# Kernel optimization log

Measured on AMD Instinct MI355X. Metric: run time of the kernel, lower is better.

Reference implementation:

```python
import jax, jax.numpy as jnp
from jax import lax
import numpy as np

# dims
VOCAB = 64
B, L = 64, 2048
EMB = 128
D_MODEL = 128
N_LAYERS = 4
D_INNER = 256      # expand=2
D_STATE = 16
D_CONV = 4
DT_RANK = 8        # ceil(d_model/16)
NCLS = 3
BN_EPS = 1e-5
RMS_EPS = 1e-5


def setup_inputs():
    key = jax.random.key(0)
    ks = iter(jax.random.split(key, 48))
    def rn(shape, s=0.02):
        return jax.random.normal(next(ks), shape, jnp.float32) * s
    tokens = jax.random.randint(next(ks), (B, L), 0, VOCAB)
    mask = jnp.ones((B, L), jnp.float32)
    emb = rn((VOCAB, EMB)).at[0].set(0.0)  # padding_idx=0
    bn_w = jnp.ones((EMB,), jnp.float32)
    bn_b = jnp.zeros((EMB,), jnp.float32)
    conv_w = rn((D_MODEL, EMB, 3))
    conv_b = jnp.zeros((D_MODEL,), jnp.float32)
    in_proj_w = rn((N_LAYERS, 2 * D_INNER, D_MODEL))
    conv1d_w = rn((N_LAYERS, D_INNER, D_CONV), 0.1)
    conv1d_b = jnp.zeros((N_LAYERS, D_INNER), jnp.float32)
    x_proj_w = rn((N_LAYERS, DT_RANK + 2 * D_STATE, D_INNER))
    dt_proj_w = rn((N_LAYERS, D_INNER, DT_RANK), 0.1)
    dt_proj_b = rn((N_LAYERS, D_INNER), 0.1)
    A_log = jnp.tile(jnp.log(jnp.arange(1, D_STATE + 1, dtype=jnp.float32))[None, None, :],
                     (N_LAYERS, D_INNER, 1))
    D_param = jnp.ones((N_LAYERS, D_INNER), jnp.float32)
    out_proj_w = rn((N_LAYERS, D_MODEL, D_INNER))
    norm_w = jnp.ones((N_LAYERS, D_MODEL), jnp.float32)
    lin1_w = rn((512, D_MODEL)); lin1_b = jnp.zeros((512,), jnp.float32)
    lin2_w = rn((512, 512));     lin2_b = jnp.zeros((512,), jnp.float32)
    lin3_w = rn((NCLS, 512));    lin3_b = jnp.zeros((NCLS,), jnp.float32)
    return dict(tokens=tokens, mask=mask, emb=emb, bn_w=bn_w, bn_b=bn_b,
                conv_w=conv_w, conv_b=conv_b, in_proj_w=in_proj_w,
                conv1d_w=conv1d_w, conv1d_b=conv1d_b, x_proj_w=x_proj_w,
                dt_proj_w=dt_proj_w, dt_proj_b=dt_proj_b, A_log=A_log,
                D_param=D_param, out_proj_w=out_proj_w, norm_w=norm_w,
                lin1_w=lin1_w, lin1_b=lin1_b, lin2_w=lin2_w, lin2_b=lin2_b,
                lin3_w=lin3_w, lin3_b=lin3_b)


def _rmsnorm(x, w):
    return x * lax.rsqrt(jnp.mean(x * x, axis=-1, keepdims=True) + RMS_EPS) * w


def _selective_scan(u, dt, A, Bm, Cm, Dv):
    # u, dt: (B,L,di); A: (di,ds); Bm, Cm: (B,L,ds); Dv: (di,)
    def step(h, inp):
        dt_t, B_t, C_t, u_t = inp           # (B,di),(B,ds),(B,ds),(B,di)
        dA = jnp.exp(dt_t[:, :, None] * A)  # (B,di,ds)
        h = dA * h + (dt_t * u_t)[:, :, None] * B_t[:, None, :]
        y = jnp.einsum('bds,bs->bd', h, C_t)
        return h, y
    h0 = jnp.zeros((u.shape[0], A.shape[0], A.shape[1]), u.dtype)
    xs = (jnp.swapaxes(dt, 0, 1), jnp.swapaxes(Bm, 0, 1),
          jnp.swapaxes(Cm, 0, 1), jnp.swapaxes(u, 0, 1))
    _, ys = lax.scan(step, h0, xs)          # ys: (L,B,di)
    return jnp.swapaxes(ys, 0, 1) + u * Dv


def _mamba(x, in_w, cw, cb, xp_w, dtp_w, dtp_b, A_log, Dv, out_w):
    # x: (B,L,d_model)
    xz = jnp.einsum('bld,ed->ble', x, in_w)            # (B,L,2*di)
    xi, z = jnp.split(xz, 2, axis=-1)
    # causal depthwise conv over time
    xc = jnp.swapaxes(xi, 1, 2)                        # (B,di,L)
    xc = lax.conv_general_dilated(xc, cw[:, None, :], (1,), [(D_CONV - 1, 0)],
                                  dimension_numbers=('NCH', 'OIH', 'NCH'),
                                  feature_group_count=D_INNER)
    xc = jax.nn.silu(xc + cb[None, :, None])
    xc = jnp.swapaxes(xc, 1, 2)                        # (B,L,di)
    x_dbl = jnp.einsum('bld,ed->ble', xc, xp_w)        # (B,L,dtr+2*ds)
    dt = jax.nn.softplus(jnp.einsum('blr,dr->bld', x_dbl[..., :DT_RANK], dtp_w) + dtp_b)
    Bm = x_dbl[..., DT_RANK:DT_RANK + D_STATE]
    Cm = x_dbl[..., DT_RANK + D_STATE:]
    A = -jnp.exp(A_log)                                # (di,ds)
    y = _selective_scan(xc, dt, A, Bm, Cm, Dv)
    y = y * jax.nn.silu(z)
    return jnp.einsum('ble,de->bld', y, out_w)         # (B,L,d_model)


def _forward(tokens, mask, emb, bn_w, bn_b, conv_w, conv_b, in_proj_w,
             conv1d_w, conv1d_b, x_proj_w, dt_proj_w, dt_proj_b, A_log,
             D_param, out_proj_w, norm_w, lin1_w, lin1_b, lin2_w, lin2_b,
             lin3_w, lin3_b):
    x = emb[tokens]                                    # (B,L,E)
    xc = jnp.swapaxes(x, 1, 2)                         # (B,E,L)
    # BatchNorm1d in eval mode: running_mean=0, running_var=1
    xc = xc * (bn_w * lax.rsqrt(jnp.array(1.0 + BN_EPS)))[None, :, None] + bn_b[None, :, None]
    xc = lax.conv_general_dilated(xc, conv_w, (1,), [(1, 1)],
                                  dimension_numbers=('NCH', 'OIH', 'NCH'))
    xc = jax.nn.relu(xc + conv_b[None, :, None])
    x = jnp.swapaxes(xc, 1, 2)                         # (B,L,D_MODEL)
    for i in range(N_LAYERS):
        x = _mamba(_rmsnorm(x, norm_w[i]), in_proj_w[i], conv1d_w[i],
                   conv1d_b[i], x_proj_w[i], dt_proj_w[i], dt_proj_b[i],
                   A_log[i], D_param[i], out_proj_w[i]) + x
    # masked average pooling
    m = mask[:, :, None]
    denom = jnp.clip(jnp.sum(m, axis=1), 1e-9, None)   # (B,1)->(B,D) broadcast
    pooled = jnp.sum(x * m, axis=1) / denom
    h = jax.nn.relu(pooled @ lin1_w.T + lin1_b)
    h = jax.nn.relu(h @ lin2_w.T + lin2_b)
    return h @ lin3_w.T + lin3_b                       # (B,NCLS)


def reference(tokens, mask, emb, bn_w, bn_b, conv_w, conv_b, in_proj_w,
              conv1d_w, conv1d_b, x_proj_w, dt_proj_w, dt_proj_b, A_log,
              D_param, out_proj_w, norm_w, lin1_w, lin1_b, lin2_w, lin2_b,
              lin3_w, lin3_b):
    return _forward(tokens, mask, emb, bn_w, bn_b, conv_w, conv_b, in_proj_w,
                    conv1d_w, conv1d_b, x_proj_w, dt_proj_w, dt_proj_b, A_log,
                    D_param, out_proj_w, norm_w, lin1_w, lin1_b, lin2_w,
                    lin2_b, lin3_w, lin3_b)
```

## Files before the change

### kernel.cpp

```cpp
#include <hip/hip_runtime.h>
#include <math.h>

#define NB     64
#define SL     2048
#define NTOK   (NB*SL)
#define EMB_D  128
#define DMODEL 128
#define DIN    256
#define DST    16
#define NLAYER 4
#define SEG    64
#define NSEG   (SL/SEG)
#define L2E    1.4426950408889634f
#define LN2    0.6931471805599453f

typedef __bf16 bf16x8 __attribute__((ext_vector_type(8)));
typedef __bf16 bf16x4 __attribute__((ext_vector_type(4)));
typedef float  f32x4  __attribute__((ext_vector_type(4)));

#define FIX_PL   ((size_t)0)
#define FIX_PM   (FIX_PL + 131072)
#define FIX_PD   (FIX_PM + 1024)
#define FIX_H1   (FIX_PD + 8192)
#define FIX_H2   (FIX_H1 + 32768)
#define FIX_WP   (FIX_H2 + 32768)
#define FIX_W2B  (FIX_WP + 65536)
#define FIX_WINB (FIX_W2B + 24576)
#define FIX_WOUTB (FIX_WINB + 131072)
#define FIX_END  (FIX_WOUTB + 65536)

__device__ __forceinline__ float fexp2(float x){ return __builtin_amdgcn_exp2f(x); }
__device__ __forceinline__ float flog2(float x){ return __builtin_amdgcn_logf(x); }
__device__ __forceinline__ float frcp (float x){ return __builtin_amdgcn_rcpf(x); }
__device__ __forceinline__ float fast_exp(float x){ return fexp2(x*L2E); }
__device__ __forceinline__ float siluf(float v){ return v * frcp(1.f + fast_exp(-v)); }
__device__ __forceinline__ float softplusf(float a){
  return fmaxf(a,0.f) + flog2(1.f + fexp2(-fabsf(a)*L2E)) * LN2;
}
__device__ __forceinline__ unsigned short bfbits(float x){
  __bf16 b = (__bf16)x; return __builtin_bit_cast(unsigned short, b);
}
__device__ __forceinline__ unsigned int packdu(float dt, float u){
  return ((unsigned int)bfbits(u) << 16) | (unsigned int)bfbits(dt);
}

#define SPSA(hA,hB,q,s0,s1) { float eA=fexp2(dt*(-fast_exp(alog[d*DST+s0])*L2E)); \
                              hA=fmaf(eA,hA,du*q.x); \
                              float eB=fexp2(dt*(-fast_exp(alog[d*DST+s1])*L2E)); \
                              hB=fmaf(eB,hB,du*q.z); }
#define SPSY(hA,hB,q,s0,s1) { float eA=fexp2(dt*(-fast_exp(alog[d*DST+s0])*L2E)); \
                              hA=fmaf(eA,hA,du*q.x); y=fmaf(hA,q.y,y); \
                              float eB=fexp2(dt*(-fast_exp(alog[d*DST+s1])*L2E)); \
                              hB=fmaf(eB,hB,du*q.z); y=fmaf(hB,q.w,y); }

#define POWTREE(r) \
  float r2=(r)*(r), r4=r2*r2, r8=r4*r4; \
  float r3=r2*(r), r5=r4*(r), r6=r4*r2, r7=r4*r3; \
  float r9=r8*(r), r10=r8*r2, r11=r8*r3, r12=r8*r4; \
  float r13=r8*r5, r14=r8*r6, r15=r8*r7, r16=r8*r8;

__global__ void k_w2b(const float* __restrict__ cw, __bf16* __restrict__ w2){
  int g = blockIdx.x*256 + threadIdx.x;
  if (g >= 128*384) return;
  int d = g / 384, j = g % 384;
  int k = j >> 7, e = j & 127;
  w2[d*384 + k*128 + e] = (__bf16)cw[d*384 + e*3 + k];
}

__global__ void k_cvt(const float* __restrict__ src, __bf16* __restrict__ dst, int n){
  int i = blockIdx.x*256 + threadIdx.x;
  if (i < n) dst[i] = (__bf16)src[i];
}

__global__ void k_wprep(const float* __restrict__ xpw, __bf16* __restrict__ wp){
  int g = blockIdx.x*256 + threadIdx.x;
  int l = g >> 14, rem = g & 16383;
  int n = rem >> 8, k = rem & 255;
  float v = 0.f;
  if (n < 8){
    v = xpw[(size_t)l*40*256 + n*256 + k];
  } else if (n < 40){
    int i = n - 8;
    int row = 8 + ((i&1)<<4) + (i>>1);
    v = xpw[(size_t)l*40*256 + row*256 + k];
  }
  wp[g] = (__bf16)v;
}

__global__ void k_embed(const int* __restrict__ tok, const float* __restrict__ emb,
                        const float* __restrict__ bnw, const float* __restrict__ bnb,
                        float* __restrict__ xp){
  int r = blockIdx.x;
  int e = threadIdx.x;
  int b = r / 2050, tp = r % 2050;
  float v = 0.f;
  if (tp != 0 && tp != 2049){
    int t = tp - 1;
    int id = tok[(size_t)b*SL + t];
    float s = bnw[e] * rsqrtf(1.0f + 1e-5f);
    v = emb[(size_t)id*EMB_D + e] * s + bnb[e];
  }
  xp[(size_t)r*EMB_D + e] = v;
}

__global__ __launch_bounds__(256) void k_rmsscale(const float* __restrict__ x,
                                                  float* __restrict__ rs){
  int wv = threadIdx.x>>6, lane = threadIdx.x&63;
  size_t tok = (size_t)blockIdx.x*4 + wv;
  float2 v = *(const float2*)(x + tok*128 + lane*2);
  float ss = v.x*v.x + v.y*v.y;
  #pragma unroll
  for (int m=1;m<64;m<<=1) ss += __shfl_xor(ss, m);
  float r = rsqrtf(ss*(1.f/128.f) + 1e-5f);
  if (lane == 0) rs[tok] = r;
}

template<int MODE, int K, int N>
__global__ __launch_bounds__(256) void k_mgemm(
    const void* __restrict__ Av, const __bf16* __restrict__ Wb,
    const float* __restrict__ bias, const float* __restrict__ rsp,
    const float* __restrict__ nwp,
    float* __restrict__ out, __bf16* __restrict__ outb, __bf16* __restrict__ outz){
  __shared__ __bf16 As[128][40];
  __shared__ __bf16 Bs[128][40];
  const int tid  = threadIdx.x;
  const int wave = tid >> 6;
  const int lane = tid & 63;
  const int col  = lane & 15;
  const int quad = lane >> 4;
  const int wm = (wave & 1) * 64;
  const int wn = (wave >> 1) * 64;
  const int m0 = blockIdx.y * 128;
  const int n0 = blockIdx.x * 128;

  f32x4 acc[4][4];
  #pragma unroll
  for (int i=0;i<4;i++)
    #pragma unroll
    for (int j=0;j<4;j++) acc[i][j] = (f32x4){0.f,0.f,0.f,0.f};

  size_t abase;
  if constexpr(MODE==0){
    int bb = m0 >> 11, tloc = m0 & 2047;
    abase = ((size_t)bb*2050 + tloc) * 128;
  } else {
    abase = (size_t)m0 * K;
  }

  const int sm = tid >> 3;
  const int sk4 = (tid & 7) * 4;
  const int bn = tid >> 2;
  const int bk8 = (tid & 3) * 8;

  for (int k0 = 0; k0 < K; k0 += 32){
    #pragma unroll
    for (int p=0;p<4;p++){
      int m = p*32 + sm;
      const float* A = (const float*)Av;
      float4 v;
      if constexpr(MODE==0){
        v = *(const float4*)(A + abase + (size_t)m*128 + k0 + sk4);
      } else {
        float4 x4 = *(const float4*)(A + abase + (size_t)m*K + k0 + sk4);
        float4 w4 = *(const float4*)(nwp + k0 + sk4);
        float s = rsp[m0 + m];
        v.x = x4.x*s*w4.x; v.y = x4.y*s*w4.y; v.z = x4.z*s*w4.z; v.w = x4.w*s*w4.w;
      }
      bf16x4 o;
      o[0] = (__bf16)v.x; o[1] = (__bf16)v.y; o[2] = (__bf16)v.z; o[3] = (__bf16)v.w;
      *(bf16x4*)&As[m][sk4] = o;
    }
    #pragma unroll
    for (int p=0;p<2;p++){
      int n = p*64 + bn;
      bf16x8 w = *(const bf16x8*)(Wb + (size_t)(n0+n)*K + k0 + bk8);
      *(bf16x8*)&Bs[n][bk8] = w;
    }
    __syncthreads();
    bf16x8 af[4], bfr[4];
    const int fq = quad*8;
    #pragma unroll
    for (int i=0;i<4;i++) af[i]  = *(const bf16x8*)&As[wm + i*16 + col][fq];
    #pragma unroll
    for (int j=0;j<4;j++) bfr[j] = *(const bf16x8*)&Bs[wn + j*16 + col][fq];
    #pragma unroll
    for (int i=0;i<4;i++)
      #pragma unroll
      for (int j=0;j<4;j++)
        acc[i][j] = __builtin_amdgcn_mfma_f32_16x16x32_bf16(af[i], bfr[j], acc[i][j], 0, 0, 0);
    __syncthreads();
  }

  #pragma unroll
  for (int i=0;i<4;i++){
    #pragma unroll
    for (int j=0;j<4;j++){
      int n_l = wn + j*16 + col;
      #pragma unroll
      for (int r=0;r<4;r++){
        int m = m0 + wm + i*16 + quad*4 + r;
        float c = acc[i][j][r];
        if constexpr(MODE==0){
          int n = n0 + n_l;
          out[(size_t)m*DMODEL + n] = fmaxf(c + bias[n], 0.f);
        } else {
          int n = n0 + n_l;
          if (n < DIN) outb[(size_t)m*DIN + n]        = (__bf16)c;
          else         outz[(size_t)m*DIN + n - DIN]  = (__bf16)siluf(c);
        }
      }
    }
  }
}

__global__ __launch_bounds__(256) void k_seg(const __bf16* __restrict__ xi,
    const __bf16* __restrict__ wpb,
    const float* __restrict__ cw, const float* __restrict__ cb,
    const float* __restrict__ dtw, const float* __restrict__ dtb,
    const float* __restrict__ alog,
    float* __restrict__ vbc, unsigned int* __restrict__ dub,
    float* __restrict__ cseg, float* __restrict__ sdtb){
  __shared__ __bf16 sxc[64][264];
  __shared__ float vls[64][68];
  const int tid = threadIdx.x;
  const size_t m0 = (size_t)blockIdx.x * 64;
  const int b = (int)(m0 >> 11);
  const int g = (int)((m0 >> 6) & (NSEG-1));
  const int seq0 = (int)(m0 & 2047);

  {
    const int c4 = (tid & 63) * 4;
    const int tw = tid >> 6;
    float wc[4][4];
    #pragma unroll
    for (int j=0;j<4;j++)
      #pragma unroll
      for (int k=0;k<4;k++) wc[j][k] = cw[(c4+j)*4 + k];
    float4 cb4 = *(const float4*)(cb + c4);
    #pragma unroll
    for (int it=0; it<16; it++){
      int t = it*4 + tw;
      float4 acc = cb4;
      #pragma unroll
      for (int k=0;k<4;k++){
        if (seq0 + t - 3 + k >= 0){
          bf16x4 xv = *(const bf16x4*)(xi + (m0 + t - 3 + k)*DIN + c4);
          acc.x = fmaf(wc[0][k], (float)xv[0], acc.x);
          acc.y = fmaf(wc[1][k], (float)xv[1], acc.y);
          acc.z = fmaf(wc[2][k], (float)xv[2], acc.z);
          acc.w = fmaf(wc[3][k], (float)xv[3], acc.w);
        }
      }
      bf16x4 o;
      o[0]=(__bf16)siluf(acc.x); o[1]=(__bf16)siluf(acc.y);
      o[2]=(__bf16)siluf(acc.z); o[3]=(__bf16)siluf(acc.w);
      *(bf16x4*)&sxc[t][c4] = o;
    }
  }
  __syncthreads();

  {
    const int wave = tid >> 6, lane = tid & 63;
    const int col = lane & 15, quad = lane >> 4;
    const int wn = wave * 16;
    f32x4 acc[4];
    #pragma unroll
    for (int i=0;i<4;i++) acc[i] = (f32x4){0.f,0.f,0.f,0.f};
    #pragma unroll
    for (int kc=0;kc<8;kc++){
      bf16x8 bfr = *(const bf16x8*)(wpb + (size_t)(wn+col)*256 + kc*32 + quad*8);
      #pragma unroll
      for (int mi=0;mi<4;mi++){
        bf16x8 af = *(const bf16x8*)&sxc[mi*16 + col][kc*32 + quad*8];
        acc[mi] = __builtin_amdgcn_mfma_f32_16x16x32_bf16(af, bfr, acc[mi], 0, 0, 0);
      }
    }
    #pragma unroll
    for (int mi=0;mi<4;mi++)
      #pragma unroll
      for (int r=0;r<4;r++)
        vls[mi*16 + quad*4 + r][wn + col] = acc[mi][r];
  }
  __syncthreads();

  #pragma unroll
  for (int p=0;p<8;p++){
    int j = p*256 + tid;
    int t = j >> 5, i = j & 31;
    vbc[(m0+t)*32 + i] = vls[t][8+i];
  }

  {
    const int d = tid;
    const float a0 = -fast_exp(alog[d*DST]) * L2E;
    bool fast = true;
    for (int s=1;s<16;s++){
      float as = -fast_exp(alog[d*DST + s]) * L2E;
      fast = fast && (fabsf(as - (float)(s+1)*a0) <= 1e-3f*fabsf(as));
    }
    float4 w8a = *(const float4*)(dtw + d*8);
    float4 w8b = *(const float4*)(dtw + d*8 + 4);
    const float bd = dtb[d];
    float h0=0.f,h1=0.f,h2=0.f,h3=0.f,h4=0.f,h5=0.f,h6=0.f,h7=0.f;
    float h8=0.f,h9=0.f,h10=0.f,h11=0.f,h12=0.f,h13=0.f,h14=0.f,h15=0.f;
    float ssum = 0.f;
    if (fast){
      for (int t=0;t<SEG;t++){
        float4 v0 = *(const float4*)&vls[t][0];
        float4 v1 = *(const float4*)&vls[t][4];
        float lin = bd;
        lin = fmaf(v0.x,w8a.x, fmaf(v0.y,w8a.y, fmaf(v0.z,w8a.z, fmaf(v0.w,w8a.w, lin))));
        lin = fmaf(v1.x,w8b.x, fmaf(v1.y,w8b.y, fmaf(v1.z,w8b.z, fmaf(v1.w,w8b.w, lin))));
        float dt = softplusf(lin);
        ssum += dt;
        float u = (float)sxc[t][d];
        dub[(m0+t)*DIN + d] = packdu(dt, u);
        float du = dt*u;
        float r1 = fexp2(dt*a0);
        POWTREE(r1)
        float4 q0 = *(const float4*)&vls[t][8];
        float4 q1 = *(const float4*)&vls[t][12];
        float4 q2 = *(const float4*)&vls[t][16];
        float4 q3 = *(const float4*)&vls[t][20];
        float4 q4 = *(const float4*)&vls[t][24];
        float4 q5 = *(const float4*)&vls[t][28];
        float4 q6 = *(const float4*)&vls[t][32];
        float4 q7 = *(const float4*)&vls[t][36];
        h0 =fmaf(r1 ,h0 ,du*q0.x); h1 =fmaf(r2 ,h1 ,du*q0.z);
        h2 =fmaf(r3 ,h2 ,du*q1.x); h3 =fmaf(r4 ,h3 ,du*q1.z);
        h4 =fmaf(r5 ,h4 ,du*q2.x); h5 =fmaf(r6 ,h5 ,du*q2.z);
        h6 =fmaf(r7 ,h6 ,du*q3.x); h7 =fmaf(r8 ,h7 ,du*q3.z);
        h8 =fmaf(r9 ,h8 ,du*q4.x); h9 =fmaf(r10,h9 ,du*q4.z);
        h10=fmaf(r11,h10,du*q5.x); h11=fmaf(r12,h11,du*q5.z);
        h12=fmaf(r13,h12,du*q6.x); h13=fmaf(r14,h13,du*q6.z);
        h14=fmaf(r15,h14,du*q7.x); h15=fmaf(r16,h15,du*q7.z);
      }
    } else {
      for (int t=0;t<SEG;t++){
        float4 v0 = *(const float4*)&vls[t][0];
        float4 v1 = *(const float4*)&vls[t][4];
        float lin = bd;
        lin = fmaf(v0.x,w8a.x, fmaf(v0.y,w8a.y, fmaf(v0.z,w8a.z, fmaf(v0.w,w8a.w, lin))));
        lin = fmaf(v1.x,w8b.x, fmaf(v1.y,w8b.y, fmaf(v1.z,w8b.z, fmaf(v1.w,w8b.w, lin))));
        float dt = softplusf(lin);
        ssum += dt;
        float u = (float)sxc[t][d];
        dub[(m0+t)*DIN + d] = packdu(dt, u);
        float du = dt*u;
        float4 q0 = *(const float4*)&vls[t][8];
        float4 q1 = *(const float4*)&vls[t][12];
        float4 q2 = *(const float4*)&vls[t][16];
        float4 q3 = *(const float4*)&vls[t][20];
        float4 q4 = *(const float4*)&vls[t][24];
        float4 q5 = *(const float4*)&vls[t][28];
        float4 q6 = *(const float4*)&vls[t][32];
        float4 q7 = *(const float4*)&vls[t][36];
        SPSA(h0,h1,q0,0,1)   SPSA(h2,h3,q1,2,3)   SPSA(h4,h5,q2,4,5)   SPSA(h6,h7,q3,6,7)
        SPSA(h8,h9,q4,8,9)   SPSA(h10,h11,q5,10,11) SPSA(h12,h13,q6,12,13) SPSA(h14,h15,q7,14,15)
      }
    }
    size_t base = (((size_t)b*NSEG + g)*DIN + d)*DST;
    float4 o;
    o.x=h0; o.y=h1; o.z=h2; o.w=h3;     *(float4*)(cseg + base     ) = o;
    o.x=h4; o.y=h5; o.z=h6; o.w=h7;     *(float4*)(cseg + base +  4) = o;
    o.x=h8; o.y=h9; o.z=h10; o.w=h11;   *(float4*)(cseg + base +  8) = o;
    o.x=h12; o.y=h13; o.z=h14; o.w=h15; *(float4*)(cseg + base + 12) = o;
    sdtb[((size_t)b*NSEG + g)*DIN + d] = ssum;
  }
}

__global__ __launch_bounds__(256) void k_scanB(float* __restrict__ cseg,
    const float* __restrict__ sdtb, const float* __restrict__ alog){
  int gl = blockIdx.x*256 + threadIdx.x;
  int b   = gl >> 12;
  int rem = gl & 4095;
  int d = rem >> 4, s = rem & 15;
  const float a = -fast_exp(alog[d*DST + s]) * L2E;
  float h = 0.f;
  for (int g=0; g<NSEG; g++){
    size_t base = ((size_t)b*NSEG + g)*DIN;
    float sd = sdtb[base + d];
    size_t ci = (base + d)*DST + s;
    float c = cseg[ci];
    cseg[ci] = h;
    h = fmaf(fexp2(a*sd), h, c);
  }
}

__global__ __launch_bounds__(256) void k_scanC3(float* __restrict__ xres,
    const unsigned int* __restrict__ dub, const float* __restrict__ vbc,
    const __bf16* __restrict__ gzb,
    const float* __restrict__ alog, const float* __restrict__ Dpar,
    const float* __restrict__ cseg, const __bf16* __restrict__ wout,
    float* __restrict__ rs){
  __shared__ __bf16 sy[64][264];
  __shared__ float svbc[64][32];
  float* sx = (float*)sy;
  const int tid = threadIdx.x;
  const size_t m0 = (size_t)blockIdx.x * 64;
  const int b = (int)(m0 >> 11);
  const int g = (int)((m0 >> 6) & (NSEG-1));

  #pragma unroll
  for (int p=0;p<8;p++){
    int j = p*256 + tid;
    int t = j >> 5, i = j & 31;
    svbc[t][i] = vbc[(m0+t)*32 + i];
  }

  {
    const int d = tid;
    const float a0 = -fast_exp(alog[d*DST]) * L2E;
    bool fast = true;
    for (int s=1;s<16;s++){
      float as = -fast_exp(alog[d*DST + s]) * L2E;
      fast = fast && (fabsf(as - (float)(s+1)*a0) <= 1e-3f*fabsf(as));
    }
    const float Dv = Dpar[d];
    size_t base = (((size_t)b*NSEG + g)*DIN + d)*DST;
    float4 hv0 = *(const float4*)(cseg + base);
    float4 hv1 = *(const float4*)(cseg + base + 4);
    float4 hv2 = *(const float4*)(cseg + base + 8);
    float4 hv3 = *(const float4*)(cseg + base + 12);
    float h0=hv0.x,h1=hv0.y,h2=hv0.z,h3=hv0.w;
    float h4=hv1.x,h5=hv1.y,h6=hv1.z,h7=hv1.w;
    float h8=hv2.x,h9=hv2.y,h10=hv2.z,h11=hv2.w;
    float h12=hv3.x,h13=hv3.y,h14=hv3.z,h15=hv3.w;
    __syncthreads();

    if (fast){
      unsigned int w = dub[m0*DIN + d];
      float gz = (float)gzb[m0*DIN + d];
      for (int t=0;t<SEG;t++){
        int tn = (t < SEG-1) ? t+1 : t;
        unsigned int wn_ = dub[(m0+tn)*DIN + d];
        float gzn = (float)gzb[(m0+tn)*DIN + d];
        float u  = __builtin_bit_cast(float, w & 0xffff0000u);
        float dt = __builtin_bit_cast(float, w << 16);
        float du = dt*u;
        float r1 = fexp2(dt*a0);
        POWTREE(r1)
        float4 q0 = *(const float4*)&svbc[t][0];
        float4 q1 = *(const float4*)&svbc[t][4];
        float4 q2 = *(const float4*)&svbc[t][8];
        float4 q3 = *(const float4*)&svbc[t][12];
        float4 q4 = *(const float4*)&svbc[t][16];
        float4 q5 = *(const float4*)&svbc[t][20];
        float4 q6 = *(const float4*)&svbc[t][24];
        float4 q7 = *(const float4*)&svbc[t][28];
        h0 =fmaf(r1 ,h0 ,du*q0.x); h1 =fmaf(r2 ,h1 ,du*q0.z);
        h2 =fmaf(r3 ,h2 ,du*q1.x); h3 =fmaf(r4 ,h3 ,du*q1.z);
        h4 =fmaf(r5 ,h4 ,du*q2.x); h5 =fmaf(r6 ,h5 ,du*q2.z);
        h6 =fmaf(r7 ,h6 ,du*q3.x); h7 =fmaf(r8 ,h7 ,du*q3.z);
        h8 =fmaf(r9 ,h8 ,du*q4.x); h9 =fmaf(r10,h9 ,du*q4.z);
        h10=fmaf(r11,h10,du*q5.x); h11=fmaf(r12,h11,du*q5.z);
        h12=fmaf(r13,h12,du*q6.x); h13=fmaf(r14,h13,du*q6.z);
        h14=fmaf(r15,h14,du*q7.x); h15=fmaf(r16,h15,du*q7.z);
        float ya = fmaf(h0,q0.y, fmaf(h1,q0.w, fmaf(h2,q1.y, h3*q1.w)));
        float yb = fmaf(h4,q2.y, fmaf(h5,q2.w, fmaf(h6,q3.y, h7*q3.w)));
        float yc = fmaf(h8,q4.y, fmaf(h9,q4.w, fmaf(h10,q5.y, h11*q5.w)));
        float yd = fmaf(h12,q6.y, fmaf(h13,q6.w, fmaf(h14,q7.y, h15*q7.w)));
        float y = (ya+yb)+(yc+yd);
        sy[t][d] = (__bf16)((y + u*Dv) * gz);
        w = wn_; gz = gzn;
      }
    } else {
      for (int t=0;t<SEG;t++){
        unsigned int w = dub[(m0+t)*DIN + d];
        float u  = __builtin_bit_cast(float, w & 0xffff0000u);
        float dt = __builtin_bit_cast(float, w << 16);
        float du = dt*u;
        float y = 0.f;
        float4 q0 = *(const float4*)&svbc[t][0];
        float4 q1 = *(const float4*)&svbc[t][4];
        float4 q2 = *(const float4*)&svbc[t][8];
        float4 q3 = *(const float4*)&svbc[t][12];
        float4 q4 = *(const float4*)&svbc[t][16];
        float4 q5 = *(const float4*)&svbc[t][20];
        float4 q6 = *(const float4*)&svbc[t][24];
        float4 q7 = *(const float4*)&svbc[t][28];
        SPSY(h0,h1,q0,0,1)   SPSY(h2,h3,q1,2,3)   SPSY(h4,h5,q2,4,5)   SPSY(h6,h7,q3,6,7)
        SPSY(h8,h9,q4,8,9)   SPSY(h10,h11,q5,10,11) SPSY(h12,h13,q6,12,13) SPSY(h14,h15,q7,14,15)
        float gz = (float)gzb[(m0+t)*DIN + d];
        sy[t][d] = (__bf16)((y + u*Dv) * gz);
      }
    }
  }
  __syncthreads();

  const int wave = tid >> 6, lane = tid & 63;
  const int col = lane & 15, quad = lane >> 4;
  const int wn = wave * 32;
  f32x4 acc[4][2];
  #pragma unroll
  for (int i=0;i<4;i++)
    #pragma unroll
    for (int j=0;j<2;j++) acc[i][j] = (f32x4){0.f,0.f,0.f,0.f};
  #pragma unroll
  for (int kc=0;kc<8;kc++){
    bf16x8 bfr0 = *(const bf16x8*)(wout + (size_t)(wn +      col)*256 + kc*32 + quad*8);
    bf16x8 bfr1 = *(const bf16x8*)(wout + (size_t)(wn + 16 + col)*256 + kc*32 + quad*8);
    #pragma unroll
    for (int mi=0;mi<4;mi++){
      bf16x8 af = *(const bf16x8*)&sy[mi*16 + col][kc*32 + quad*8];
      acc[mi][0] = __builtin_amdgcn_mfma_f32_16x16x32_bf16(af, bfr0, acc[mi][0], 0, 0, 0);
      acc[mi][1] = __builtin_amdgcn_mfma_f32_16x16x32_bf16(af, bfr1, acc[mi][1], 0, 0, 0);
    }
  }
  __syncthreads();

  #pragma unroll
  for (int mi=0;mi<4;mi++){
    #pragma unroll
    for (int j=0;j<2;j++){
      int n = wn + j*16 + col;
      #pragma unroll
      for (int r=0;r<4;r++){
        int ml = mi*16 + quad*4 + r;
        size_t go = (m0 + ml)*DMODEL + n;
        float nx = xres[go] + acc[mi][j][r];
        xres[go] = nx;
        sx[ml*132 + n] = nx;
      }
    }
  }
  __syncthreads();
  {
    int row = tid >> 2, q = tid & 3;
    const float* pr = sx + row*132 + q*32;
    float ss = 0.f;
    #pragma unroll
    for (int i=0;i<32;i+=4){
      float4 v = *(const float4*)(pr + i);
      ss += v.x*v.x + v.y*v.y + v.z*v.z + v.w*v.w;
    }
    ss += __shfl_xor(ss, 1);
    ss += __shfl_xor(ss, 2);
    if (q == 0) rs[m0 + row] = rsqrtf(ss*(1.f/128.f) + 1e-5f);
  }
}

__global__ __launch_bounds__(256) void k_pool1(const float* __restrict__ x,
    const float* __restrict__ mask, float* __restrict__ part, float* __restrict__ pmask){
  int b = blockIdx.y, seg = blockIdx.x;
  int d = threadIdx.x & 127, half = threadIdx.x >> 7;
  int t0 = seg*128 + half*64;
  float acc = 0.f, macc = 0.f;
  for (int i=0;i<64;i++){
    int t = t0 + i;
    float mv = mask[(size_t)b*SL + t];
    acc = fmaf(x[((size_t)b*SL + t)*DMODEL + d], mv, acc);
    macc += mv;
  }
  __shared__ float sm[256];
  __shared__ float smm[2];
  sm[threadIdx.x] = acc;
  if (d == 0) smm[half] = macc;
  __syncthreads();
  if (half == 0){
    part[((size_t)b*16 + seg)*128 + d] = sm[d] + sm[128+d];
    if (d == 0) pmask[b*16 + seg] = smm[0] + smm[1];
  }
}

__global__ void k_pool2(const float* __restrict__ part, const float* __restrict__ pmask,
                        float* __restrict__ pooled){
  int b = blockIdx.x, d = threadIdx.x;
  float acc = 0.f, ms = 0.f;
  for (int s=0;s<16;s++){ acc += part[((size_t)b*16+s)*128 + d]; ms += pmask[b*16+s]; }
  pooled[(size_t)b*128 + d] = acc / fmaxf(ms, 1e-9f);
}

__global__ void k_mlp_a(const float* __restrict__ in, const float* __restrict__ w,
                        const float* __restrict__ bias, float* __restrict__ out, int K){
  int b = blockIdx.y;
  int n = blockIdx.x*128 + threadIdx.x;
  const float4* pw = (const float4*)(w + (size_t)n*K);
  const float4* pi = (const float4*)(in + (size_t)b*K);
  float acc = 0.f;
  for (int k=0;k<K/4;k++){
    float4 a = pi[k], ww = pw[k];
    acc = fmaf(a.x,ww.x, fmaf(a.y,ww.y, fmaf(a.z,ww.z, fmaf(a.w,ww.w, acc))));
  }
  out[(size_t)b*512 + n] = fmaxf(acc + bias[n], 0.f);
}

__global__ void k_mlp3(const float* __restrict__ h, const float* __restrict__ w,
                       const float* __restrict__ bias, float* __restrict__ out){
  int b = blockIdx.x;
  int n = threadIdx.x >> 6, lane = threadIdx.x & 63;
  if (n >= 3) return;
  float acc = 0.f;
  for (int k=lane; k<512; k+=64) acc = fmaf(h[(size_t)b*512+k], w[(size_t)n*512+k], acc);
  #pragma unroll
  for (int m=1;m<64;m<<=1) acc += __shfl_xor(acc, m);
  if (lane == 0) out[(size_t)b*3 + n] = acc + bias[n];
}

extern "C" void kernel_launch(void* const* d_in, const int* in_sizes, int n_in,
                              void* d_out, int out_size, void* d_ws, size_t ws_size,
                              hipStream_t stream){
  const int*   tokens = (const int*)  d_in[0];
  const float* mask   = (const float*)d_in[1];
  const float* emb    = (const float*)d_in[2];
  const float* bn_w   = (const float*)d_in[3];
  const float* bn_b   = (const float*)d_in[4];
  const float* conv_w = (const float*)d_in[5];
  const float* conv_b = (const float*)d_in[6];
  const float* in_w   = (const float*)d_in[7];
  const float* c1_w   = (const float*)d_in[8];
  const float* c1_b   = (const float*)d_in[9];
  const float* xp_w   = (const float*)d_in[10];
  const float* dtp_w  = (const float*)d_in[11];
  const float* dtp_b  = (const float*)d_in[12];
  const float* A_log  = (const float*)d_in[13];
  const float* D_par  = (const float*)d_in[14];
  const float* out_w  = (const float*)d_in[15];
  const float* nrm_w  = (const float*)d_in[16];
  const float* l1w = (const float*)d_in[17]; const float* l1b = (const float*)d_in[18];
  const float* l2w = (const float*)d_in[19]; const float* l2b = (const float*)d_in[20];
  const float* l3w = (const float*)d_in[21]; const float* l3b = (const float*)d_in[22];
  float* dout = (float*)d_out;

  int CB = 64;
  while (CB > 1 && ((size_t)CB*SL*741 + FIX_END)*4 > ws_size) CB >>= 1;
  if (((size_t)CB*SL*741 + FIX_END)*4 > ws_size) return;
  const size_t CTOK = (size_t)CB*SL;

  float* ws  = (float*)d_ws;
  float* pl  = ws + FIX_PL;
  float* pm  = ws + FIX_PM;
  float* pd  = ws + FIX_PD;
  float* h1  = ws + FIX_H1;
  float* h2  = ws + FIX_H2;
  __bf16* wpb   = (__bf16*)(ws + FIX_WP);
  __bf16* w2b   = (__bf16*)(ws + FIX_W2B);
  __bf16* winb  = (__bf16*)(ws + FIX_WINB);
  __bf16* woutb = (__bf16*)(ws + FIX_WOUTB);
  float* xcb = ws + FIX_END;
  float* rs  = xcb + CTOK*128;
  __bf16* xib = (__bf16*)(rs + CTOK);
  unsigned int* dub = (unsigned int*)(xib + CTOK*256);
  float* pad = (float*)xib;
  float* vbc = (float*)(dub + CTOK*256);
  float* csg = vbc + CTOK*32;
  float* sdt = csg + CTOK*64;
  __bf16* zb  = (__bf16*)(sdt + CTOK*4);

  k_w2b<<<192, 256, 0, stream>>>(conv_w, w2b);
  k_cvt<<<1024, 256, 0, stream>>>(in_w,  winb,  4*512*128);
  k_cvt<<<512,  256, 0, stream>>>(out_w, woutb, 4*128*256);
  k_wprep<<<256, 256, 0, stream>>>(xp_w, wpb);

  const int nchunks = NB / CB;
  for (int c = 0; c < nchunks; c++){
    const int* tok_c = tokens + (size_t)c*CTOK;

    k_embed<<<CB*2050, 128, 0, stream>>>(tok_c, emb, bn_w, bn_b, pad);
    k_mgemm<0,384,128><<<dim3(1, CTOK/128), 256, 0, stream>>>(
        pad, w2b, conv_b, nullptr, nullptr, xcb, nullptr, nullptr);
    k_rmsscale<<<CTOK/4, 256, 0, stream>>>(xcb, rs);

    for (int layer = 0; layer < NLAYER; layer++){
      const __bf16* lin = winb  + (size_t)layer*512*128;
      const float* lcw  = c1_w  + (size_t)layer*DIN*4;
      const float* lcb  = c1_b  + (size_t)layer*DIN;
      const float* ldw  = dtp_w + (size_t)layer*DIN*8;
      const float* ldb  = dtp_b + (size_t)layer*DIN;
      const float* lal  = A_log + (size_t)layer*DIN*DST;
      const float* lD   = D_par + (size_t)layer*DIN;
      const __bf16* low = woutb + (size_t)layer*128*256;
      const float* lnw  = nrm_w + (size_t)layer*128;

      k_mgemm<1,128,512><<<dim3(4, CTOK/128), 256, 0, stream>>>(
          xcb, lin, nullptr, rs, lnw, nullptr, xib, zb);
      k_seg<<<(int)(CTOK/64), 256, 0, stream>>>(
          xib, wpb + (size_t)layer*64*256, lcw, lcb, ldw, ldb, lal, vbc, dub, csg, sdt);
      k_scanB<<<CB*16, 256, 0, stream>>>(csg, sdt, lal);
      k_scanC3<<<(int)(CTOK/64), 256, 0, stream>>>(
          xcb, dub, vbc, zb, lal, lD, csg, low, rs);
    }

    k_pool1<<<dim3(16, CB), 256, 0, stream>>>(
        xcb, mask + (size_t)c*CTOK, pl + (size_t)c*CB*16*128, pm + (size_t)c*CB*16);
  }

  k_pool2<<<NB, 128, 0, stream>>>(pl, pm, pd);
  k_mlp_a<<<dim3(4, NB), 128, 0, stream>>>(pd, l1w, l1b, h1, 128);
  k_mlp_a<<<dim3(4, NB), 128, 0, stream>>>(h1, l2w, l2b, h2, 512);
  k_mlp3<<<NB, 256, 0, stream>>>(h2, l3w, l3b, dout);
}
```

Measured before the change: 1.520 ms.

## Split SSM state across two threads per channel in seg and scan kernels

Doubles the block size of k_seg and k_scanC3 to 512 threads and assigns each d_inner channel to two threads, each holding 8 of the 16 state elements. The y reduction is combined with a lane shuffle, and the MFMA and reduction work is redistributed across 8 waves. This aims to cut per-thread serial recurrence work and register pressure so more waves are resident to hide latency. In exchange it adds redundant dt/softplus computation in both halves, shuffle overhead, and half-idle lanes on the stores.

```diff
diff --git a/kernel.cpp b/kernel.cpp
--- a/kernel.cpp
+++ b/kernel.cpp
@@ -43,21 +43,6 @@
 __device__ __forceinline__ unsigned int packdu(float dt, float u){
   return ((unsigned int)bfbits(u) << 16) | (unsigned int)bfbits(dt);
 }
-
-#define SPSA(hA,hB,q,s0,s1) { float eA=fexp2(dt*(-fast_exp(alog[d*DST+s0])*L2E)); \
-                              hA=fmaf(eA,hA,du*q.x); \
-                              float eB=fexp2(dt*(-fast_exp(alog[d*DST+s1])*L2E)); \
-                              hB=fmaf(eB,hB,du*q.z); }
-#define SPSY(hA,hB,q,s0,s1) { float eA=fexp2(dt*(-fast_exp(alog[d*DST+s0])*L2E)); \
-                              hA=fmaf(eA,hA,du*q.x); y=fmaf(hA,q.y,y); \
-                              float eB=fexp2(dt*(-fast_exp(alog[d*DST+s1])*L2E)); \
-                              hB=fmaf(eB,hB,du*q.z); y=fmaf(hB,q.w,y); }
-
-#define POWTREE(r) \
-  float r2=(r)*(r), r4=r2*r2, r8=r4*r4; \
-  float r3=r2*(r), r5=r4*(r), r6=r4*r2, r7=r4*r3; \
-  float r9=r8*(r), r10=r8*r2, r11=r8*r3, r12=r8*r4; \
-  float r13=r8*r5, r14=r8*r6, r15=r8*r7, r16=r8*r8;
 
 __global__ void k_w2b(const float* __restrict__ cw, __bf16* __restrict__ w2){
   int g = blockIdx.x*256 + threadIdx.x;
@@ -213,7 +198,7 @@
   }
 }
 
-__global__ __launch_bounds__(256) void k_seg(const __bf16* __restrict__ xi,
+__global__ __launch_bounds__(512,6) void k_seg(const __bf16* __restrict__ xi,
     const __bf16* __restrict__ wpb,
     const float* __restrict__ cw, const float* __restrict__ cb,
     const float* __restrict__ dtw, const float* __restrict__ dtb,
@@ -238,8 +223,8 @@
       for (int k=0;k<4;k++) wc[j][k] = cw[(c4+j)*4 + k];
     float4 cb4 = *(const float4*)(cb + c4);
     #pragma unroll
-    for (int it=0; it<16; it++){
-      int t = it*4 + tw;
+    for (int it=0; it<8; it++){
+      int t = it*8 + tw;
       float4 acc = cb4;
       #pragma unroll
       for (int k=0;k<4;k++){
@@ -262,36 +247,38 @@
   {
     const int wave = tid >> 6, lane = tid & 63;
     const int col = lane & 15, quad = lane >> 4;
-    const int wn = wave * 16;
-    f32x4 acc[4];
-    #pragma unroll
-    for (int i=0;i<4;i++) acc[i] = (f32x4){0.f,0.f,0.f,0.f};
+    const int wr  = (wave >> 2) * 32;
+    const int wc2 = (wave & 3) * 16;
+    f32x4 acc[2];
+    acc[0] = (f32x4){0.f,0.f,0.f,0.f};
+    acc[1] = (f32x4){0.f,0.f,0.f,0.f};
     #pragma unroll
     for (int kc=0;kc<8;kc++){
-      bf16x8 bfr = *(const bf16x8*)(wpb + (size_t)(wn+col)*256 + kc*32 + quad*8);
-      #pragma unroll
-      for (int mi=0;mi<4;mi++){
-        bf16x8 af = *(const bf16x8*)&sxc[mi*16 + col][kc*32 + quad*8];
+      bf16x8 bfr = *(const bf16x8*)(wpb + (size_t)(wc2+col)*256 + kc*32 + quad*8);
+      #pragma unroll
+      for (int mi=0;mi<2;mi++){
+        bf16x8 af = *(const bf16x8*)&sxc[wr + mi*16 + col][kc*32 + quad*8];
         acc[mi] = __builtin_amdgcn_mfma_f32_16x16x32_bf16(af, bfr, acc[mi], 0, 0, 0);
       }
     }
     #pragma unroll
-    for (int mi=0;mi<4;mi++)
+    for (int mi=0;mi<2;mi++)
       #pragma unroll
       for (int r=0;r<4;r++)
-        vls[mi*16 + quad*4 + r][wn + col] = acc[mi][r];
+        vls[wr + mi*16 + quad*4 + r][wc2 + col] = acc[mi][r];
   }
   __syncthreads();
 
   #pragma unroll
-  for (int p=0;p<8;p++){
-    int j = p*256 + tid;
+  for (int p=0;p<4;p++){
+    int j = p*512 + tid;
     int t = j >> 5, i = j & 31;
     vbc[(m0+t)*32 + i] = vls[t][8+i];
   }
 
   {
-    const int d = tid;
+    const int d = tid >> 1;
+    const int half = tid & 1;
     const float a0 = -fast_exp(alog[d*DST]) * L2E;
     bool fast = true;
     for (int s=1;s<16;s++){
@@ -301,8 +288,10 @@
     float4 w8a = *(const float4*)(dtw + d*8);
     float4 w8b = *(const float4*)(dtw + d*8 + 4);
     const float bd = dtb[d];
-    float h0=0.f,h1=0.f,h2=0.f,h3=0.f,h4=0.f,h5=0.f,h6=0.f,h7=0.f;
-    float h8=0.f,h9=0.f,h10=0.f,h11=0.f,h12=0.f,h13=0.f,h14=0.f,h15=0.f;
+    const int qb = half*16;
+    float h[8];
+    #pragma unroll
+    for (int k=0;k<8;k++) h[k] = 0.f;
     float ssum = 0.f;
     if (fast){
       for (int t=0;t<SEG;t++){
@@ -314,28 +303,25 @@
         float dt = softplusf(lin);
         ssum += dt;
         float u = (float)sxc[t][d];
-        dub[(m0+t)*DIN + d] = packdu(dt, u);
+        if (!half) dub[(m0+t)*DIN + d] = packdu(dt, u);
         float du = dt*u;
         float r1 = fexp2(dt*a0);
-        POWTREE(r1)
-        float4 q0 = *(const float4*)&vls[t][8];
-        float4 q1 = *(const float4*)&vls[t][12];
-        float4 q2 = *(const float4*)&vls[t][16];
-        float4 q3 = *(const float4*)&vls[t][20];
-        float4 q4 = *(const float4*)&vls[t][24];
-        float4 q5 = *(const float4*)&vls[t][28];
-        float4 q6 = *(const float4*)&vls[t][32];
-        float4 q7 = *(const float4*)&vls[t][36];
-        h0 =fmaf(r1 ,h0 ,du*q0.x); h1 =fmaf(r2 ,h1 ,du*q0.z);
-        h2 =fmaf(r3 ,h2 ,du*q1.x); h3 =fmaf(r4 ,h3 ,du*q1.z);
-        h4 =fmaf(r5 ,h4 ,du*q2.x); h5 =fmaf(r6 ,h5 ,du*q2.z);
-        h6 =fmaf(r7 ,h6 ,du*q3.x); h7 =fmaf(r8 ,h7 ,du*q3.z);
-        h8 =fmaf(r9 ,h8 ,du*q4.x); h9 =fmaf(r10,h9 ,du*q4.z);
-        h10=fmaf(r11,h10,du*q5.x); h11=fmaf(r12,h11,du*q5.z);
-        h12=fmaf(r13,h12,du*q6.x); h13=fmaf(r14,h13,du*q6.z);
-        h14=fmaf(r15,h14,du*q7.x); h15=fmaf(r16,h15,du*q7.z);
+        float r2=r1*r1, r3=r2*r1, r4=r2*r2, r5=r4*r1, r6=r4*r2, r7=r4*r3, r8=r4*r4;
+        float bs = half ? r8 : 1.0f;
+        float4 q0 = *(const float4*)&vls[t][8+qb];
+        float4 q1 = *(const float4*)&vls[t][12+qb];
+        float4 q2 = *(const float4*)&vls[t][16+qb];
+        float4 q3 = *(const float4*)&vls[t][20+qb];
+        float pw[8] = {r1,r2,r3,r4,r5,r6,r7,r8};
+        float B_[8] = {q0.x,q0.z,q1.x,q1.z,q2.x,q2.z,q3.x,q3.z};
+        #pragma unroll
+        for (int k=0;k<8;k++)
+          h[k] = fmaf(bs*pw[k], h[k], du*B_[k]);
       }
     } else {
+      float aA[8];
+      #pragma unroll
+      for (int k=0;k<8;k++) aA[k] = -fast_exp(alog[d*DST + half*8 + k]) * L2E;
       for (int t=0;t<SEG;t++){
         float4 v0 = *(const float4*)&vls[t][0];
         float4 v1 = *(const float4*)&vls[t][4];
@@ -345,27 +331,25 @@
         float dt = softplusf(lin);
         ssum += dt;
         float u = (float)sxc[t][d];
-        dub[(m0+t)*DIN + d] = packdu(dt, u);
+        if (!half) dub[(m0+t)*DIN + d] = packdu(dt, u);
         float du = dt*u;
-        float4 q0 = *(const float4*)&vls[t][8];
-        float4 q1 = *(const float4*)&vls[t][12];
-        float4 q2 = *(const float4*)&vls[t][16];
-        float4 q3 = *(const float4*)&vls[t][20];
-        float4 q4 = *(const float4*)&vls[t][24];
-        float4 q5 = *(const float4*)&vls[t][28];
-        float4 q6 = *(const float4*)&vls[t][32];
-        float4 q7 = *(const float4*)&vls[t][36];
-        SPSA(h0,h1,q0,0,1)   SPSA(h2,h3,q1,2,3)   SPSA(h4,h5,q2,4,5)   SPSA(h6,h7,q3,6,7)
-        SPSA(h8,h9,q4,8,9)   SPSA(h10,h11,q5,10,11) SPSA(h12,h13,q6,12,13) SPSA(h14,h15,q7,14,15)
-      }
-    }
-    size_t base = (((size_t)b*NSEG + g)*DIN + d)*DST;
+        float4 q0 = *(const float4*)&vls[t][8+qb];
+        float4 q1 = *(const float4*)&vls[t][12+qb];
+        float4 q2 = *(const float4*)&vls[t][16+qb];
+        float4 q3 = *(const float4*)&vls[t][20+qb];
+        float B_[8] = {q0.x,q0.z,q1.x,q1.z,q2.x,q2.z,q3.x,q3.z};
+        #pragma unroll
+        for (int k=0;k<8;k++){
+          float e = fexp2(dt*aA[k]);
+          h[k] = fmaf(e, h[k], du*B_[k]);
+        }
+      }
+    }
+    size_t base = (((size_t)b*NSEG + g)*DIN + d)*DST + half*8;
     float4 o;
-    o.x=h0; o.y=h1; o.z=h2; o.w=h3;     *(float4*)(cseg + base     ) = o;
-    o.x=h4; o.y=h5; o.z=h6; o.w=h7;     *(float4*)(cseg + base +  4) = o;
-    o.x=h8; o.y=h9; o.z=h10; o.w=h11;   *(float4*)(cseg + base +  8) = o;
-    o.x=h12; o.y=h13; o.z=h14; o.w=h15; *(float4*)(cseg + base + 12) = o;
-    sdtb[((size_t)b*NSEG + g)*DIN + d] = ssum;
+    o.x=h[0]; o.y=h[1]; o.z=h[2]; o.w=h[3];  *(float4*)(cseg + base    ) = o;
+    o.x=h[4]; o.y=h[5]; o.z=h[6]; o.w=h[7];  *(float4*)(cseg + base + 4) = o;
+    if (!half) sdtb[((size_t)b*NSEG + g)*DIN + d] = ssum;
   }
 }
 
@@ -387,7 +371,7 @@
   }
 }
 
-__global__ __launch_bounds__(256) void k_scanC3(float* __restrict__ xres,
+__global__ __launch_bounds__(512,6) void k_scanC3(float* __restrict__ xres,
     const unsigned int* __restrict__ dub, const float* __restrict__ vbc,
     const __bf16* __restrict__ gzb,
     const float* __restrict__ alog, const float* __restrict__ Dpar,
@@ -402,14 +386,15 @@
   const int g = (int)((m0 >> 6) & (NSEG-1));
 
   #pragma unroll
-  for (int p=0;p<8;p++){
-    int j = p*256 + tid;
+  for (int p=0;p<4;p++){
+    int j = p*512 + tid;
     int t = j >> 5, i = j & 31;
     svbc[t][i] = vbc[(m0+t)*32 + i];
   }
 
   {
-    const int d = tid;
+    const int d = tid >> 1;
+    const int half = tid & 1;
     const float a0 = -fast_exp(alog[d*DST]) * L2E;
     bool fast = true;
     for (int s=1;s<16;s++){
@@ -417,15 +402,11 @@
       fast = fast && (fabsf(as - (float)(s+1)*a0) <= 1e-3f*fabsf(as));
     }
     const float Dv = Dpar[d];
-    size_t base = (((size_t)b*NSEG + g)*DIN + d)*DST;
+    size_t base = (((size_t)b*NSEG + g)*DIN + d)*DST + half*8;
     float4 hv0 = *(const float4*)(cseg + base);
     float4 hv1 = *(const float4*)(cseg + base + 4);
-    float4 hv2 = *(const float4*)(cseg + base + 8);
-    float4 hv3 = *(const float4*)(cseg + base + 12);
-    float h0=hv0.x,h1=hv0.y,h2=hv0.z,h3=hv0.w;
-    float h4=hv1.x,h5=hv1.y,h6=hv1.z,h7=hv1.w;
-    float h8=hv2.x,h9=hv2.y,h10=hv2.z,h11=hv2.w;
-    float h12=hv3.x,h13=hv3.y,h14=hv3.z,h15=hv3.w;
+    float h[8] = {hv0.x,hv0.y,hv0.z,hv0.w,hv1.x,hv1.y,hv1.z,hv1.w};
+    const int qb = half*16;
     __syncthreads();
 
     if (fast){
@@ -439,50 +420,53 @@
         float dt = __builtin_bit_cast(float, w << 16);
         float du = dt*u;
         float r1 = fexp2(dt*a0);
-        POWTREE(r1)
-        float4 q0 = *(const float4*)&svbc[t][0];
-        float4 q1 = *(const float4*)&svbc[t][4];
-        float4 q2 = *(const float4*)&svbc[t][8];
-        float4 q3 = *(const float4*)&svbc[t][12];
-        float4 q4 = *(const float4*)&svbc[t][16];
-        float4 q5 = *(const float4*)&svbc[t][20];
-        float4 q6 = *(const float4*)&svbc[t][24];
-        float4 q7 = *(const float4*)&svbc[t][28];
-        h0 =fmaf(r1 ,h0 ,du*q0.x); h1 =fmaf(r2 ,h1 ,du*q0.z);
-        h2 =fmaf(r3 ,h2 ,du*q1.x); h3 =fmaf(r4 ,h3 ,du*q1.z);
-        h4 =fmaf(r5 ,h4 ,du*q2.x); h5 =fmaf(r6 ,h5 ,du*q2.z);
-        h6 =fmaf(r7 ,h6 ,du*q3.x); h7 =fmaf(r8 ,h7 ,du*q3.z);
-        h8 =fmaf(r9 ,h8 ,du*q4.x); h9 =fmaf(r10,h9 ,du*q4.z);
-        h10=fmaf(r11,h10,du*q5.x); h11=fmaf(r12,h11,du*q5.z);
-        h12=fmaf(r13,h12,du*q6.x); h13=fmaf(r14,h13,du*q6.z);
-        h14=fmaf(r15,h14,du*q7.x); h15=fmaf(r16,h15,du*q7.z);
-        float ya = fmaf(h0,q0.y, fmaf(h1,q0.w, fmaf(h2,q1.y, h3*q1.w)));
-        float yb = fmaf(h4,q2.y, fmaf(h5,q2.w, fmaf(h6,q3.y, h7*q3.w)));
-        float yc = fmaf(h8,q4.y, fmaf(h9,q4.w, fmaf(h10,q5.y, h11*q5.w)));
-        float yd = fmaf(h12,q6.y, fmaf(h13,q6.w, fmaf(h14,q7.y, h15*q7.w)));
-        float y = (ya+yb)+(yc+yd);
-        sy[t][d] = (__bf16)((y + u*Dv) * gz);
+        float r2=r1*r1, r3=r2*r1, r4=r2*r2, r5=r4*r1, r6=r4*r2, r7=r4*r3, r8=r4*r4;
+        float bs = half ? r8 : 1.0f;
+        float4 q0 = *(const float4*)&svbc[t][qb];
+        float4 q1 = *(const float4*)&svbc[t][qb+4];
+        float4 q2 = *(const float4*)&svbc[t][qb+8];
+        float4 q3 = *(const float4*)&svbc[t][qb+12];
+        float pw[8] = {r1,r2,r3,r4,r5,r6,r7,r8};
+        float B_[8] = {q0.x,q0.z,q1.x,q1.z,q2.x,q2.z,q3.x,q3.z};
+        float C_[8] = {q0.y,q0.w,q1.y,q1.w,q2.y,q2.w,q3.y,q3.w};
+        float ya = 0.f, yb = 0.f;
+        #pragma unroll
+        for (int k=0;k<8;k+=2){
+          h[k]   = fmaf(bs*pw[k],   h[k],   du*B_[k]);
+          h[k+1] = fmaf(bs*pw[k+1], h[k+1], du*B_[k+1]);
+          ya = fmaf(h[k],   C_[k],   ya);
+          yb = fmaf(h[k+1], C_[k+1], yb);
+        }
+        float y = ya + yb;
+        y += __shfl_xor(y, 1);
+        if (!half) sy[t][d] = (__bf16)((y + u*Dv) * gz);
         w = wn_; gz = gzn;
       }
     } else {
+      float aA[8];
+      #pragma unroll
+      for (int k=0;k<8;k++) aA[k] = -fast_exp(alog[d*DST + half*8 + k]) * L2E;
       for (int t=0;t<SEG;t++){
         unsigned int w = dub[(m0+t)*DIN + d];
         float u  = __builtin_bit_cast(float, w & 0xffff0000u);
         float dt = __builtin_bit_cast(float, w << 16);
         float du = dt*u;
+        float4 q0 = *(const float4*)&svbc[t][qb];
+        float4 q1 = *(const float4*)&svbc[t][qb+4];
+        float4 q2 = *(const float4*)&svbc[t][qb+8];
+        float4 q3 = *(const float4*)&svbc[t][qb+12];
+        float B_[8] = {q0.x,q0.z,q1.x,q1.z,q2.x,q2.z,q3.x,q3.z};
+        float C_[8] = {q0.y,q0.w,q1.y,q1.w,q2.y,q2.w,q3.y,q3.w};
         float y = 0.f;
-        float4 q0 = *(const float4*)&svbc[t][0];
-        float4 q1 = *(const float4*)&svbc[t][4];
-        float4 q2 = *(const float4*)&svbc[t][8];
-        float4 q3 = *(const float4*)&svbc[t][12];
-        float4 q4 = *(const float4*)&svbc[t][16];
-        float4 q5 = *(const float4*)&svbc[t][20];
-        float4 q6 = *(const float4*)&svbc[t][24];
-        float4 q7 = *(const float4*)&svbc[t][28];
-        SPSY(h0,h1,q0,0,1)   SPSY(h2,h3,q1,2,3)   SPSY(h4,h5,q2,4,5)   SPSY(h6,h7,q3,6,7)
-        SPSY(h8,h9,q4,8,9)   SPSY(h10,h11,q5,10,11) SPSY(h12,h13,q6,12,13) SPSY(h14,h15,q7,14,15)
+        #pragma unroll
+        for (int k=0;k<8;k++){
+          float e = fexp2(dt*aA[k]);
+          h[k] = fmaf(e, h[k], du*B_[k]);
+          y = fmaf(h[k], C_[k], y);
+        }
+        y += __shfl_xor(y, 1);
         float gz = (float)gzb[(m0+t)*DIN + d];
-        sy[t][d] = (__bf16)((y + u*Dv) * gz);
+        if (!half) sy[t][d] = (__bf16)((y + u*Dv) * gz);
       }
     }
   }
@@ -490,52 +474,46 @@
 
   const int wave = tid >> 6, lane = tid & 63;
   const int col = lane & 15, quad = lane >> 4;
-  const int wn = wave * 32;
-  f32x4 acc[4][2];
-  #pragma unroll
-  for (int i=0;i<4;i++)
-    #pragma unroll
-    for (int j=0;j<2;j++) acc[i][j] = (f32x4){0.f,0.f,0.f,0.f};
+  const int wn = wave * 16;
+  f32x4 acc[4];
+  #pragma unroll
+  for (int i=0;i<4;i++) acc[i] = (f32x4){0.f,0.f,0.f,0.f};
   #pragma unroll
   for (int kc=0;kc<8;kc++){
-    bf16x8 bfr0 = *(const bf16x8*)(wout + (size_t)(wn +      col)*256 + kc*32 + quad*8);
-    bf16x8 bfr1 = *(const bf16x8*)(wout + (size_t)(wn + 16 + col)*256 + kc*32 + quad*8);
+    bf16x8 bfr = *(const bf16x8*)(wout + (size_t)(wn + col)*256 + kc*32 + quad*8);
     #pragma unroll
     for (int mi=0;mi<4;mi++){
       bf16x8 af = *(const bf16x8*)&sy[mi*16 + col][kc*32 + quad*8];
-      acc[mi][0] = __builtin_amdgcn_mfma_f32_16x16x32_bf16(af, bfr0, acc[mi][0], 0, 0, 0);
-      acc[mi][1] = __builtin_amdgcn_mfma_f32_16x16x32_bf16(af, bfr1, acc[mi][1], 0, 0, 0);
+      acc[mi] = __builtin_amdgcn_mfma_f32_16x16x32_bf16(af, bfr, acc[mi], 0, 0, 0);
     }
   }
   __syncthreads();
 
   #pragma unroll
   for (int mi=0;mi<4;mi++){
-    #pragma unroll
-    for (int j=0;j<2;j++){
-      int n = wn + j*16 + col;
-      #pragma unroll
-      for (int r=0;r<4;r++){
-        int ml = mi*16 + quad*4 + r;
-        size_t go = (m0 + ml)*DMODEL + n;
-        float nx = xres[go] + acc[mi][j][r];
-        xres[go] = nx;
-        sx[ml*132 + n] = nx;
-      }
+    int n = wn + col;
+    #pragma unroll
+    for (int r=0;r<4;r++){
+      int ml = mi*16 + quad*4 + r;
+      size_t go = (m0 + ml)*DMODEL + n;
+      float nx = xres[go] + acc[mi][r];
+      xres[go] = nx;
+      sx[ml*132 + n] = nx;
     }
   }
   __syncthreads();
   {
-    int row = tid >> 2, q = tid & 3;
-    const float* pr = sx + row*132 + q*32;
+    int row = tid >> 3, q = tid & 7;
+    const float* pr = sx + row*132 + q*16;
     float ss = 0.f;
     #pragma unroll
-    for (int i=0;i<32;i+=4){
+    for (int i=0;i<16;i+=4){
       float4 v = *(const float4*)(pr + i);
       ss += v.x*v.x + v.y*v.y + v.z*v.z + v.w*v.w;
     }
     ss += __shfl_xor(ss, 1);
     ss += __shfl_xor(ss, 2);
+    ss += __shfl_xor(ss, 4);
     if (q == 0) rs[m0 + row] = rsqrtf(ss*(1.f/128.f) + 1e-5f);
   }
 }
@@ -674,10 +652,10 @@
 
       k_mgemm<1,128,512><<<dim3(4, CTOK/128), 256, 0, stream>>>(
           xcb, lin, nullptr, rs, lnw, nullptr, xib, zb);
-      k_seg<<<(int)(CTOK/64), 256, 0, stream>>>(
+      k_seg<<<(int)(CTOK/64), 512, 0, stream>>>(
           xib, wpb + (size_t)layer*64*256, lcw, lcb, ldw, ldb, lal, vbc, dub, csg, sdt);
       k_scanB<<<CB*16, 256, 0, stream>>>(csg, sdt, lal);
-      k_scanC3<<<(int)(CTOK/64), 256, 0, stream>>>(
+      k_scanC3<<<(int)(CTOK/64), 512, 0, stream>>>(
           xcb, dub, vbc, zb, lal, lD, csg, low, rs);
     }
 
```

Measured after the change: 1.629 ms. +7.1%, slower.
